# Optimization experiments

Measured on AMD Instinct MI355X. Metric: run time of the kernel, lower is better.

The kernel has to match this reference:

```python
import jax, jax.numpy as jnp
import numpy as np

VOCAB, D_MODEL, NHEAD, NLAYER, DIM_FF, MAX_LEN = 32000, 1024, 16, 6, 4096, 1024
B, L = 8, 1024
PAD_ID = 0
EPS = 1e-5


def _ln(x, g, b):
    m = x.mean(-1, keepdims=True)
    v = x.var(-1, keepdims=True)
    return (x - m) / jnp.sqrt(v + EPS) * g + b


def _mha(x, Wqkv, bqkv, Wo, bo, kpm):
    # x: [B,L,D]; Wqkv: [3D,D]; kpm: [B,L] bool (True = padded key)
    Bx, Lx, D = x.shape
    dh = D // NHEAD
    qkv = x @ Wqkv.T + bqkv                       # [B,L,3D]
    q, k, v = jnp.split(qkv, 3, axis=-1)
    sp = lambda t: t.reshape(Bx, Lx, NHEAD, dh).transpose(0, 2, 1, 3)  # [B,H,L,dh]
    q, k, v = sp(q), sp(k), sp(v)
    scores = jnp.einsum('bhqd,bhkd->bhqk', q, k) * (dh ** -0.5)
    scores = jnp.where(kpm[:, None, None, :], jnp.asarray(-1e9, scores.dtype), scores)
    attn = jax.nn.softmax(scores, axis=-1)        # explicit weights, as ForceWeightsMHA demands
    o = jnp.einsum('bhqk,bhkd->bhqd', attn, v)
    o = o.transpose(0, 2, 1, 3).reshape(Bx, Lx, D)
    return o @ Wo.T + bo


def setup_inputs() -> dict:
    key = jax.random.key(0)
    ks = jax.random.split(key, 20)
    s = 0.02
    n = lambda k, shp: (jax.random.normal(k, shp, dtype=jnp.float32) * s)
    inp = {
        'input_ids': jax.random.randint(ks[0], (B, L), 0, VOCAB, dtype=jnp.int64) if jax.config.jax_enable_x64 else jax.random.randint(ks[0], (B, L), 0, VOCAB).astype(jnp.int32),
        'tok_emb': n(ks[1], (VOCAB, D_MODEL)),
        'pos_emb': n(ks[2], (MAX_LEN, D_MODEL)),
        'Wqkv': n(ks[3], (NLAYER, 3 * D_MODEL, D_MODEL)),
        'bqkv': jnp.zeros((NLAYER, 3 * D_MODEL), jnp.float32),
        'Wo': n(ks[4], (NLAYER, D_MODEL, D_MODEL)),
        'bo': jnp.zeros((NLAYER, D_MODEL), jnp.float32),
        'ln1_g': jnp.ones((NLAYER, D_MODEL), jnp.float32),
        'ln1_b': jnp.zeros((NLAYER, D_MODEL), jnp.float32),
        'W1': n(ks[5], (NLAYER, DIM_FF, D_MODEL)),
        'b1': jnp.zeros((NLAYER, DIM_FF), jnp.float32),
        'W2': n(ks[6], (NLAYER, D_MODEL, DIM_FF)),
        'b2': jnp.zeros((NLAYER, D_MODEL), jnp.float32),
        'ln2_g': jnp.ones((NLAYER, D_MODEL), jnp.float32),
        'ln2_b': jnp.zeros((NLAYER, D_MODEL), jnp.float32),
        'head_ln_g': jnp.ones((D_MODEL,), jnp.float32),
        'head_ln_b': jnp.zeros((D_MODEL,), jnp.float32),
        'head_W': n(ks[7], (MAX_LEN, D_MODEL)),
        'head_b': jnp.zeros((MAX_LEN,), jnp.float32),
    }
    return inp


def reference(input_ids, tok_emb, pos_emb, Wqkv, bqkv, Wo, bo, ln1_g, ln1_b,
              W1, b1, W2, b2, ln2_g, ln2_b, head_ln_g, head_ln_b, head_W, head_b):
    Bx, Lx = input_ids.shape
    x = tok_emb[input_ids] + pos_emb[None, :Lx]           # [B,L,D]
    kpm = (input_ids == PAD_ID).at[:, 0].set(False)        # key padding mask, col 0 forced valid
    for i in range(NLAYER):                                # post-norm encoder layer (PyTorch default)
        x = _ln(x + _mha(x, Wqkv[i], bqkv[i], Wo[i], bo[i], kpm), ln1_g[i], ln1_b[i])
        ff = jax.nn.gelu(x @ W1[i].T + b1[i], approximate=False) @ W2[i].T + b2[i]
        x = _ln(x + ff, ln2_g[i], ln2_b[i])
    cls = x[:, 0, :]                                       # [B,D]
    return _ln(cls, head_ln_g, head_ln_b) @ head_W.T + head_b  # [B,MAX_LEN]
```

## Files before the change

kernel.cpp:

```cpp
#include <hip/hip_runtime.h>
#include <cstdint>

#define D_MODEL 1024
#define NHEAD   16
#define NLAYER  6
#define DIM_FF  4096
#define SEQ_B   8
#define SEQ_L   1024
#define TOKENS  (SEQ_B*SEQ_L)

typedef __bf16 v8bf __attribute__((ext_vector_type(8)));
typedef float  v4f  __attribute__((ext_vector_type(4)));

__device__ __forceinline__ unsigned short f2bf(float f) {
  unsigned int u = __float_as_uint(f);
  u += 0x7fffu + ((u >> 16) & 1u);
  return (unsigned short)(u >> 16);
}

__device__ __forceinline__ void gl_lds16(const void* g, void* l) {
  __builtin_amdgcn_global_load_lds(
      (const __attribute__((address_space(1))) void*)g,
      (__attribute__((address_space(3))) void*)l, 16, 0, 0);
}

__global__ __launch_bounds__(256) void f2b_kernel(const float* __restrict__ in,
                                                  unsigned short* __restrict__ out, long n) {
  long i = (long)blockIdx.x * 256 + threadIdx.x;
  long stride = (long)gridDim.x * 256;
  for (; i < n; i += stride) out[i] = f2bf(in[i]);
}

__global__ __launch_bounds__(256) void embed_kernel(const int* __restrict__ ids,
    const float* __restrict__ tok, const float* __restrict__ pos,
    float* __restrict__ X, unsigned short* __restrict__ Xb) {
  long i = (long)blockIdx.x * 256 + threadIdx.x;
  int d = (int)(i & (D_MODEL - 1));
  long bl = i >> 10;
  int l = (int)(bl & (SEQ_L - 1));
  int id = ids[bl];
  float v = tok[(long)id * D_MODEL + d] + pos[(long)l * D_MODEL + d];
  X[i] = v; Xb[i] = f2bf(v);
}

template<int EPI>
__global__ __launch_bounds__(256) void gemm128(
    const unsigned short* __restrict__ A,
    const unsigned short* __restrict__ W,
    const float* __restrict__ bias,
    float* __restrict__ Cf, unsigned short* __restrict__ Cb,
    unsigned short* __restrict__ Vt,
    int M, int N, int K) {
  __shared__ unsigned short As[128 * 32];
  __shared__ unsigned short Bs[128 * 32];
  int tid = threadIdx.x;
  int wave = tid >> 6, lane = tid & 63;
  int l15 = lane & 15, quad = lane >> 4;
  int m0 = blockIdx.y * 128, n0 = blockIdx.x * 128;
  int wm = (wave >> 1) * 64, wn = (wave & 1) * 64;

  int srow = tid >> 2, sc8 = (tid & 3) << 3;
  const unsigned short* Ag0 = A + (long)(m0 + srow) * K + sc8;
  const unsigned short* Ag1 = A + (long)(m0 + srow + 64) * K + sc8;
  const unsigned short* Wg0 = W + (long)(n0 + srow) * K + sc8;
  const unsigned short* Wg1 = W + (long)(n0 + srow + 64) * K + sc8;
  unsigned short* As0 = As + tid * 8;
  unsigned short* As1 = As + tid * 8 + 2048;
  unsigned short* Bs0 = Bs + tid * 8;
  unsigned short* Bs1 = Bs + tid * 8 + 2048;

  v4f acc[4][4];
  #pragma unroll
  for (int i = 0; i < 4; ++i)
    #pragma unroll
    for (int j = 0; j < 4; ++j) acc[i][j] = (v4f){0.f, 0.f, 0.f, 0.f};

  int ksteps = K >> 5;
  for (int ks = 0; ks < ksteps; ++ks) {
    int k0 = ks << 5;
    __syncthreads();
    gl_lds16(Ag0 + k0, As0);
    gl_lds16(Ag1 + k0, As1);
    gl_lds16(Wg0 + k0, Bs0);
    gl_lds16(Wg1 + k0, Bs1);
    __syncthreads();
    v8bf af[4], bf[4];
    #pragma unroll
    for (int i = 0; i < 4; ++i)
      af[i] = *(const v8bf*)&As[(wm + i * 16 + l15) * 32 + quad * 8];
    #pragma unroll
    for (int j = 0; j < 4; ++j)
      bf[j] = *(const v8bf*)&Bs[(wn + j * 16 + l15) * 32 + quad * 8];
    #pragma unroll
    for (int i = 0; i < 4; ++i)
      #pragma unroll
      for (int j = 0; j < 4; ++j)
        acc[i][j] = __builtin_amdgcn_mfma_f32_16x16x32_bf16(af[i], bf[j], acc[i][j], 0, 0, 0);
  }

  #pragma unroll
  for (int i = 0; i < 4; ++i) {
    int crow0 = m0 + wm + i * 16 + quad * 4;
    #pragma unroll
    for (int j = 0; j < 4; ++j) {
      int col = n0 + wn + j * 16 + l15;
      float bv = bias[col];
      if (EPI == 3 && col >= 2048) {
        int hc = (col - 2048) >> 6, d = (col - 2048) & 63;
        int bb = crow0 >> 10, l = crow0 & 1023;
        ushort4 pk;
        pk.x = f2bf(acc[i][j][0] + bv);
        pk.y = f2bf(acc[i][j][1] + bv);
        pk.z = f2bf(acc[i][j][2] + bv);
        pk.w = f2bf(acc[i][j][3] + bv);
        *(ushort4*)&Vt[((long)((bb * 16 + hc) * 64 + d)) * 1024 + l] = pk;
      } else {
        #pragma unroll
        for (int r = 0; r < 4; ++r) {
          float v = acc[i][j][r] + bv;
          if (EPI == 1) v = 0.5f * v * (1.f + erff(v * 0.70710678118f));
          long idx = (long)(crow0 + r) * N + col;
          if (EPI == 0) Cf[idx] = v;
          else          Cb[idx] = f2bf(v);
        }
      }
    }
  }
}

#define KP 72
__global__ __launch_bounds__(256) void attn2(
    const unsigned short* __restrict__ QKVb,
    const unsigned short* __restrict__ Vtg,
    const int* __restrict__ ids,
    unsigned short* __restrict__ Ob) {
  __shared__ unsigned short Ks[64 * KP];
  __shared__ unsigned short Vs[64 * KP];
  __shared__ unsigned short Ps[4][16 * KP];
  int tid = threadIdx.x, wave = tid >> 6, lane = tid & 63;
  int l15 = lane & 15, quad = lane >> 4;
  int b = blockIdx.z, h = blockIdx.y, q0 = blockIdx.x * 64;

  int qrow = q0 + wave * 16 + l15;
  const unsigned short* qb = QKVb + (long)(b * 1024 + qrow) * 3072 + h * 64;
  v8bf gq0 = *(const v8bf*)(qb + quad * 8);
  v8bf gq1 = *(const v8bf*)(qb + 32 + quad * 8);

  float m_run[4], l_run[4];
  v4f O[4];
  #pragma unroll
  for (int r = 0; r < 4; ++r) { m_run[r] = -1e30f; l_run[r] = 0.f; }
  #pragma unroll
  for (int j = 0; j < 4; ++j) O[j] = (v4f){0.f, 0.f, 0.f, 0.f};

  const unsigned short* kgb = QKVb + (long)b * 1024 * 3072 + 1024 + h * 64;
  const unsigned short* vgb = Vtg + (long)((b * 16 + h) * 64) * 1024;
  const int* idrow = ids + b * 1024;

  for (int k0 = 0; k0 < SEQ_L; k0 += 64) {
    __syncthreads();
    #pragma unroll
    for (int it = 0; it < 2; ++it) {
      int f = it * 256 + tid;
      int row = f >> 3, e8 = (f & 7) << 3;
      v8bf kv = *(const v8bf*)(kgb + (long)(k0 + row) * 3072 + e8);
      *(v8bf*)&Ks[row * KP + e8] = kv;
      v8bf vv = *(const v8bf*)(vgb + (long)row * 1024 + k0 + e8);
      *(v8bf*)&Vs[row * KP + e8] = vv;
    }
    __syncthreads();

    float p[4][4], mr[4];
    #pragma unroll
    for (int r = 0; r < 4; ++r) mr[r] = -1e30f;
    #pragma unroll
    for (int t = 0; t < 4; ++t) {
      v8bf kf0 = *(const v8bf*)&Ks[(t * 16 + l15) * KP + quad * 8];
      v8bf kf1 = *(const v8bf*)&Ks[(t * 16 + l15) * KP + 32 + quad * 8];
      v4f s = (v4f){0.f, 0.f, 0.f, 0.f};
      s = __builtin_amdgcn_mfma_f32_16x16x32_bf16(gq0, kf0, s, 0, 0, 0);
      s = __builtin_amdgcn_mfma_f32_16x16x32_bf16(gq1, kf1, s, 0, 0, 0);
      int kg = k0 + t * 16 + l15;
      bool msk = (idrow[kg] == 0) && (kg != 0);
      #pragma unroll
      for (int r = 0; r < 4; ++r) {
        float sv = msk ? -1e9f : s[r] * 0.125f;
        p[t][r] = sv;
        mr[r] = fmaxf(mr[r], sv);
      }
    }
    #pragma unroll
    for (int r = 0; r < 4; ++r) {
      mr[r] = fmaxf(mr[r], __shfl_xor(mr[r], 1, 64));
      mr[r] = fmaxf(mr[r], __shfl_xor(mr[r], 2, 64));
      mr[r] = fmaxf(mr[r], __shfl_xor(mr[r], 4, 64));
      mr[r] = fmaxf(mr[r], __shfl_xor(mr[r], 8, 64));
    }
    float alpha[4], ls[4];
    #pragma unroll
    for (int r = 0; r < 4; ++r) {
      float mn = fmaxf(m_run[r], mr[r]);
      alpha[r] = __expf(m_run[r] - mn);
      m_run[r] = mn; ls[r] = 0.f;
    }
    #pragma unroll
    for (int t = 0; t < 4; ++t)
      #pragma unroll
      for (int r = 0; r < 4; ++r) {
        p[t][r] = __expf(p[t][r] - m_run[r]);
        ls[r] += p[t][r];
      }
    #pragma unroll
    for (int r = 0; r < 4; ++r) {
      ls[r] += __shfl_xor(ls[r], 1, 64);
      ls[r] += __shfl_xor(ls[r], 2, 64);
      ls[r] += __shfl_xor(ls[r], 4, 64);
      ls[r] += __shfl_xor(ls[r], 8, 64);
      l_run[r] = l_run[r] * alpha[r] + ls[r];
    }
    #pragma unroll
    for (int j = 0; j < 4; ++j)
      #pragma unroll
      for (int r = 0; r < 4; ++r) O[j][r] *= alpha[r];

    #pragma unroll
    for (int t = 0; t < 4; ++t)
      #pragma unroll
      for (int r = 0; r < 4; ++r)
        Ps[wave][(quad * 4 + r) * KP + t * 16 + l15] = f2bf(p[t][r]);
    v8bf pa0 = *(const v8bf*)&Ps[wave][l15 * KP + quad * 8];
    v8bf pa1 = *(const v8bf*)&Ps[wave][l15 * KP + 32 + quad * 8];
    #pragma unroll
    for (int j = 0; j < 4; ++j) {
      v8bf vf0 = *(const v8bf*)&Vs[(j * 16 + l15) * KP + quad * 8];
      v8bf vf1 = *(const v8bf*)&Vs[(j * 16 + l15) * KP + 32 + quad * 8];
      O[j] = __builtin_amdgcn_mfma_f32_16x16x32_bf16(pa0, vf0, O[j], 0, 0, 0);
      O[j] = __builtin_amdgcn_mfma_f32_16x16x32_bf16(pa1, vf1, O[j], 0, 0, 0);
    }
  }

  int qd = q0 + wave * 16 + quad * 4;
  #pragma unroll
  for (int r = 0; r < 4; ++r) {
    float inv = 1.f / l_run[r];
    #pragma unroll
    for (int j = 0; j < 4; ++j)
      Ob[(long)(b * 1024 + qd + r) * 1024 + h * 64 + j * 16 + l15] = f2bf(O[j][r] * inv);
  }
}

__global__ __launch_bounds__(256) void add_ln(
    const float* __restrict__ Xin, const float* __restrict__ Yin,
    const float* __restrict__ g, const float* __restrict__ bta,
    float* __restrict__ outF, unsigned short* __restrict__ outB,
    long in_stride, long out_stride) {
  int row = blockIdx.x;
  const float* x = Xin + (long)row * in_stride;
  const float* y = Yin ? Yin + (long)row * 1024 : nullptr;
  int tid = threadIdx.x;
  float v[4];
  float s = 0.f, s2 = 0.f;
  #pragma unroll
  for (int j = 0; j < 4; ++j) {
    int d = j * 256 + tid;
    float t = x[d] + (y ? y[d] : 0.f);
    v[j] = t; s += t; s2 += t * t;
  }
  __shared__ float red[8];
  int lane = tid & 63, wave = tid >> 6;
  #pragma unroll
  for (int o = 32; o > 0; o >>= 1) { s += __shfl_down(s, o, 64); s2 += __shfl_down(s2, o, 64); }
  if (lane == 0) { red[wave] = s; red[4 + wave] = s2; }
  __syncthreads();
  s  = red[0] + red[1] + red[2] + red[3];
  s2 = red[4] + red[5] + red[6] + red[7];
  float mean = s * (1.f / 1024.f);
  float var  = s2 * (1.f / 1024.f) - mean * mean;
  float rstd = rsqrtf(var + 1e-5f);
  float* of = outF + (long)row * out_stride;
  unsigned short* ob = outB ? outB + (long)row * out_stride : nullptr;
  #pragma unroll
  for (int j = 0; j < 4; ++j) {
    int d = j * 256 + tid;
    float o = (v[j] - mean) * rstd * g[d] + bta[d];
    of[d] = o;
    if (ob) ob[d] = f2bf(o);
  }
}

__global__ __launch_bounds__(256) void head_kernel(
    const float* __restrict__ cls, const float* __restrict__ hW,
    const float* __restrict__ hb, float* __restrict__ out) {
  int n = blockIdx.x * 256 + threadIdx.x;
  int b = blockIdx.y;
  const float4* c4 = (const float4*)(cls + b * 1024);
  const float4* w4 = (const float4*)(hW + (long)n * 1024);
  float s = 0.f;
  #pragma unroll 8
  for (int d = 0; d < 256; ++d) {
    float4 a = c4[d], w = w4[d];
    s += a.x * w.x + a.y * w.y + a.z * w.z + a.w * w.w;
  }
  out[b * 1024 + n] = s + hb[n];
}

extern "C" void kernel_launch(void* const* d_in, const int* in_sizes, int n_in,
                              void* d_out, int out_size, void* d_ws, size_t ws_size,
                              hipStream_t stream) {
  const int*   ids  = (const int*)d_in[0];
  const float* tok  = (const float*)d_in[1];
  const float* pos  = (const float*)d_in[2];
  const float* Wqkv = (const float*)d_in[3];
  const float* bqkv = (const float*)d_in[4];
  const float* Wo   = (const float*)d_in[5];
  const float* bo   = (const float*)d_in[6];
  const float* ln1g = (const float*)d_in[7];
  const float* ln1b = (const float*)d_in[8];
  const float* W1   = (const float*)d_in[9];
  const float* b1   = (const float*)d_in[10];
  const float* W2   = (const float*)d_in[11];
  const float* b2   = (const float*)d_in[12];
  const float* ln2g = (const float*)d_in[13];
  const float* ln2b = (const float*)d_in[14];
  const float* hlng = (const float*)d_in[15];
  const float* hlnb = (const float*)d_in[16];
  const float* hW   = (const float*)d_in[17];
  const float* hb   = (const float*)d_in[18];
  float* out = (float*)d_out;

  char* ws = (char*)d_ws;
  size_t off = 0;
  auto alloc = [&](size_t bytes) {
    char* p = ws + off;
    off = (off + bytes + 255) & ~(size_t)255;
    return p;
  };
  unsigned short* Wqkv_b = (unsigned short*)alloc((size_t)NLAYER*3072*1024*2);
  unsigned short* Wo_b   = (unsigned short*)alloc((size_t)NLAYER*1024*1024*2);
  unsigned short* W1_b   = (unsigned short*)alloc((size_t)NLAYER*4096*1024*2);
  unsigned short* W2_b   = (unsigned short*)alloc((size_t)NLAYER*1024*4096*2);
  float*          X      = (float*)alloc((size_t)TOKENS*1024*4);
  unsigned short* Xb     = (unsigned short*)alloc((size_t)TOKENS*1024*2);
  unsigned short* Qb     = (unsigned short*)alloc((size_t)TOKENS*3072*2);
  unsigned short* Vtg    = (unsigned short*)alloc((size_t)TOKENS*1024*2);
  float*          Y      = (float*)alloc((size_t)TOKENS*1024*4);
  unsigned short* Ab     = (unsigned short*)alloc((size_t)TOKENS*1024*2);
  unsigned short* Gb     = Qb;
  float*          cls    = (float*)alloc(8*1024*4);

  f2b_kernel<<<2048, 256, 0, stream>>>(Wqkv, Wqkv_b, (long)NLAYER*3072*1024);
  f2b_kernel<<<2048, 256, 0, stream>>>(Wo,   Wo_b,   (long)NLAYER*1024*1024);
  f2b_kernel<<<2048, 256, 0, stream>>>(W1,   W1_b,   (long)NLAYER*4096*1024);
  f2b_kernel<<<2048, 256, 0, stream>>>(W2,   W2_b,   (long)NLAYER*1024*4096);
  embed_kernel<<<(TOKENS*1024)/256, 256, 0, stream>>>(ids, tok, pos, X, Xb);

  for (int i = 0; i < NLAYER; ++i) {
    gemm128<3><<<dim3(3072/128, TOKENS/128), 256, 0, stream>>>(
        Xb, Wqkv_b + (size_t)i*3072*1024, bqkv + i*3072, nullptr, Qb, Vtg, TOKENS, 3072, 1024);
    attn2<<<dim3(SEQ_L/64, NHEAD, SEQ_B), 256, 0, stream>>>(Qb, Vtg, ids, Ab);
    gemm128<0><<<dim3(1024/128, TOKENS/128), 256, 0, stream>>>(
        Ab, Wo_b + (size_t)i*1024*1024, bo + i*1024, Y, nullptr, nullptr, TOKENS, 1024, 1024);
    add_ln<<<TOKENS, 256, 0, stream>>>(X, Y, ln1g + i*1024, ln1b + i*1024, X, Xb, 1024L, 1024L);
    gemm128<1><<<dim3(4096/128, TOKENS/128), 256, 0, stream>>>(
        Xb, W1_b + (size_t)i*4096*1024, b1 + i*4096, nullptr, Gb, nullptr, TOKENS, 4096, 1024);
    gemm128<0><<<dim3(1024/128, TOKENS/128), 256, 0, stream>>>(
        Gb, W2_b + (size_t)i*1024*4096, b2 + i*1024, Y, nullptr, nullptr, TOKENS, 1024, 4096);
    add_ln<<<TOKENS, 256, 0, stream>>>(X, Y, ln2g + i*1024, ln2b + i*1024, X, Xb, 1024L, 1024L);
  }
  add_ln<<<8, 256, 0, stream>>>(X, nullptr, hlng, hlnb, cls, nullptr, (long)SEQ_L*1024, 1024L);
  head_kernel<<<dim3(4, 8), 256, 0, stream>>>(cls, hW, hb, out);
}
```

Measured before the change: 3.407 ms.

## Swizzle LDS tiles, remap GEMM blocks per XCD, streamline attention softmax

Applies an XOR swizzle to the GEMM A/B shared-memory tiles to avoid bank conflicts. It also remaps GEMM block indices so that each XCD works on a contiguous group of M tiles, for better L2 reuse. Attention now loads K/V straight into swizzled LDS with global_load_lds instead of a padded register copy. It precomputes an additive float mask bias and folds the softmax scale into an exp2 argument. The per-row probability sum is computed with an MFMA against a ones vector instead of shuffle reductions. Conversion and embedding kernels are vectorised to float4, and native bf16 conversions replace the manual rounding routine. The remap hardcodes the 64-tile M dimension, and the ones-MFMA row sum adds matrix work and a shuffle per tile.

```diff
diff --git a/kernel.cpp b/kernel.cpp
--- a/kernel.cpp
+++ b/kernel.cpp
@@ -9,14 +9,9 @@
 #define SEQ_L   1024
 #define TOKENS  (SEQ_B*SEQ_L)
 
-typedef __bf16 v8bf __attribute__((ext_vector_type(8)));
-typedef float  v4f  __attribute__((ext_vector_type(4)));
-
-__device__ __forceinline__ unsigned short f2bf(float f) {
-  unsigned int u = __float_as_uint(f);
-  u += 0x7fffu + ((u >> 16) & 1u);
-  return (unsigned short)(u >> 16);
-}
+typedef __bf16 v8bf  __attribute__((ext_vector_type(8)));
+typedef __bf16 v4bf  __attribute__((ext_vector_type(4)));
+typedef float  v4f   __attribute__((ext_vector_type(4)));
 
 __device__ __forceinline__ void gl_lds16(const void* g, void* l) {
   __builtin_amdgcn_global_load_lds(
@@ -24,23 +19,37 @@
       (__attribute__((address_space(3))) void*)l, 16, 0, 0);
 }
 
-__global__ __launch_bounds__(256) void f2b_kernel(const float* __restrict__ in,
-                                                  unsigned short* __restrict__ out, long n) {
+__global__ __launch_bounds__(256) void f2b_kernel(const float4* __restrict__ in,
+                                                  ushort4* __restrict__ out, long n4) {
   long i = (long)blockIdx.x * 256 + threadIdx.x;
   long stride = (long)gridDim.x * 256;
-  for (; i < n; i += stride) out[i] = f2bf(in[i]);
+  for (; i < n4; i += stride) {
+    float4 v = in[i];
+    v4bf r = { (__bf16)v.x, (__bf16)v.y, (__bf16)v.z, (__bf16)v.w };
+    out[i] = *(ushort4*)&r;
+  }
 }
 
 __global__ __launch_bounds__(256) void embed_kernel(const int* __restrict__ ids,
-    const float* __restrict__ tok, const float* __restrict__ pos,
-    float* __restrict__ X, unsigned short* __restrict__ Xb) {
+    const float4* __restrict__ tok, const float4* __restrict__ pos,
+    float4* __restrict__ X, ushort4* __restrict__ Xb) {
   long i = (long)blockIdx.x * 256 + threadIdx.x;
-  int d = (int)(i & (D_MODEL - 1));
-  long bl = i >> 10;
+  int d4 = (int)(i & 255);
+  long bl = i >> 8;
   int l = (int)(bl & (SEQ_L - 1));
   int id = ids[bl];
-  float v = tok[(long)id * D_MODEL + d] + pos[(long)l * D_MODEL + d];
-  X[i] = v; Xb[i] = f2bf(v);
+  float4 t = tok[(long)id * 256 + d4];
+  float4 p = pos[(long)l * 256 + d4];
+  float4 v = {t.x + p.x, t.y + p.y, t.z + p.z, t.w + p.w};
+  X[i] = v;
+  v4bf r = { (__bf16)v.x, (__bf16)v.y, (__bf16)v.z, (__bf16)v.w };
+  Xb[i] = *(ushort4*)&r;
+}
+
+__global__ __launch_bounds__(256) void maskb_kernel(const int* __restrict__ ids,
+                                                    float* __restrict__ mb) {
+  int i = blockIdx.x * 256 + threadIdx.x;
+  mb[i] = (ids[i] == 0 && (i & 1023) != 0) ? -1e9f : 0.f;
 }
 
 template<int EPI>
@@ -56,10 +65,17 @@
   int tid = threadIdx.x;
   int wave = tid >> 6, lane = tid & 63;
   int l15 = lane & 15, quad = lane >> 4;
-  int m0 = blockIdx.y * 128, n0 = blockIdx.x * 128;
+
+  int id = blockIdx.y * gridDim.x + blockIdx.x;
+  int xcd = id & 7, sidx = id >> 3;
+  int mt = xcd * 8 + (sidx & 7);
+  int nt = sidx >> 3;
+  int m0 = mt * 128, n0 = nt * 128;
   int wm = (wave >> 1) * 64, wn = (wave & 1) * 64;
 
-  int srow = tid >> 2, sc8 = (tid & 3) << 3;
+  int srow = tid >> 2;
+  int ssl  = (tid & 3) ^ ((srow >> 1) & 3);
+  int sc8  = ssl << 3;
   const unsigned short* Ag0 = A + (long)(m0 + srow) * K + sc8;
   const unsigned short* Ag1 = A + (long)(m0 + srow + 64) * K + sc8;
   const unsigned short* Wg0 = W + (long)(n0 + srow) * K + sc8;
@@ -68,6 +84,16 @@
   unsigned short* As1 = As + tid * 8 + 2048;
   unsigned short* Bs0 = Bs + tid * 8;
   unsigned short* Bs1 = Bs + tid * 8 + 2048;
+
+  const unsigned short* afp[4];
+  const unsigned short* bfp[4];
+  #pragma unroll
+  for (int i = 0; i < 4; ++i) {
+    int r = wm + i * 16 + l15;
+    afp[i] = &As[r * 32 + ((quad ^ ((r >> 1) & 3)) << 3)];
+    int rb = wn + i * 16 + l15;
+    bfp[i] = &Bs[rb * 32 + ((quad ^ ((rb >> 1) & 3)) << 3)];
+  }
 
   v4f acc[4][4];
   #pragma unroll
@@ -86,11 +112,9 @@
     __syncthreads();
     v8bf af[4], bf[4];
     #pragma unroll
-    for (int i = 0; i < 4; ++i)
-      af[i] = *(const v8bf*)&As[(wm + i * 16 + l15) * 32 + quad * 8];
-    #pragma unroll
-    for (int j = 0; j < 4; ++j)
-      bf[j] = *(const v8bf*)&Bs[(wn + j * 16 + l15) * 32 + quad * 8];
+    for (int i = 0; i < 4; ++i) af[i] = *(const v8bf*)afp[i];
+    #pragma unroll
+    for (int j = 0; j < 4; ++j) bf[j] = *(const v8bf*)bfp[j];
     #pragma unroll
     for (int i = 0; i < 4; ++i)
       #pragma unroll
@@ -108,12 +132,9 @@
       if (EPI == 3 && col >= 2048) {
         int hc = (col - 2048) >> 6, d = (col - 2048) & 63;
         int bb = crow0 >> 10, l = crow0 & 1023;
-        ushort4 pk;
-        pk.x = f2bf(acc[i][j][0] + bv);
-        pk.y = f2bf(acc[i][j][1] + bv);
-        pk.z = f2bf(acc[i][j][2] + bv);
-        pk.w = f2bf(acc[i][j][3] + bv);
-        *(ushort4*)&Vt[((long)((bb * 16 + hc) * 64 + d)) * 1024 + l] = pk;
+        v4bf pk = { (__bf16)(acc[i][j][0] + bv), (__bf16)(acc[i][j][1] + bv),
+                    (__bf16)(acc[i][j][2] + bv), (__bf16)(acc[i][j][3] + bv) };
+        *(ushort4*)&Vt[((long)((bb * 16 + hc) * 64 + d)) * 1024 + l] = *(ushort4*)&pk;
       } else {
         #pragma unroll
         for (int r = 0; r < 4; ++r) {
@@ -121,22 +142,22 @@
           if (EPI == 1) v = 0.5f * v * (1.f + erff(v * 0.70710678118f));
           long idx = (long)(crow0 + r) * N + col;
           if (EPI == 0) Cf[idx] = v;
-          else          Cb[idx] = f2bf(v);
+          else          ((__bf16*)Cb)[idx] = (__bf16)v;
         }
       }
     }
   }
 }
 
-#define KP 72
+#define PSP 72
 __global__ __launch_bounds__(256) void attn2(
     const unsigned short* __restrict__ QKVb,
     const unsigned short* __restrict__ Vtg,
-    const int* __restrict__ ids,
+    const float* __restrict__ mb,
     unsigned short* __restrict__ Ob) {
-  __shared__ unsigned short Ks[64 * KP];
-  __shared__ unsigned short Vs[64 * KP];
-  __shared__ unsigned short Ps[4][16 * KP];
+  __shared__ unsigned short Ks[64 * 64];
+  __shared__ unsigned short Vs[64 * 64];
+  __shared__ unsigned short Ps[4][16 * PSP];
   int tid = threadIdx.x, wave = tid >> 6, lane = tid & 63;
   int l15 = lane & 15, quad = lane >> 4;
   int b = blockIdx.z, h = blockIdx.y, q0 = blockIdx.x * 64;
@@ -146,6 +167,10 @@
   v8bf gq0 = *(const v8bf*)(qb + quad * 8);
   v8bf gq1 = *(const v8bf*)(qb + 32 + quad * 8);
 
+  v8bf bones;
+  #pragma unroll
+  for (int j = 0; j < 8; ++j) bones[j] = (l15 == 0) ? (__bf16)1.0f : (__bf16)0.0f;
+
   float m_run[4], l_run[4];
   v4f O[4];
   #pragma unroll
@@ -155,19 +180,20 @@
 
   const unsigned short* kgb = QKVb + (long)b * 1024 * 3072 + 1024 + h * 64;
   const unsigned short* vgb = Vtg + (long)((b * 16 + h) * 64) * 1024;
-  const int* idrow = ids + b * 1024;
+  const float* mrow = mb + b * 1024;
+
+  int srow = tid >> 3;
+  int ssl  = (tid & 7) ^ (srow & 7);
+  int ph0 = (quad ^ (l15 & 7)) << 3;
+  int ph1 = ((quad + 4) ^ (l15 & 7)) << 3;
+  const float SC = 0.18033688011112042f;
 
   for (int k0 = 0; k0 < SEQ_L; k0 += 64) {
     __syncthreads();
-    #pragma unroll
-    for (int it = 0; it < 2; ++it) {
-      int f = it * 256 + tid;
-      int row = f >> 3, e8 = (f & 7) << 3;
-      v8bf kv = *(const v8bf*)(kgb + (long)(k0 + row) * 3072 + e8);
-      *(v8bf*)&Ks[row * KP + e8] = kv;
-      v8bf vv = *(const v8bf*)(vgb + (long)row * 1024 + k0 + e8);
-      *(v8bf*)&Vs[row * KP + e8] = vv;
-    }
+    gl_lds16(kgb + (long)(k0 + srow) * 3072 + ssl * 8, &Ks[tid * 8]);
+    gl_lds16(kgb + (long)(k0 + srow + 32) * 3072 + ssl * 8, &Ks[tid * 8 + 2048]);
+    gl_lds16(vgb + (long)srow * 1024 + k0 + ssl * 8, &Vs[tid * 8]);
+    gl_lds16(vgb + (long)(srow + 32) * 1024 + k0 + ssl * 8, &Vs[tid * 8 + 2048]);
     __syncthreads();
 
     float p[4][4], mr[4];
@@ -175,16 +201,16 @@
     for (int r = 0; r < 4; ++r) mr[r] = -1e30f;
     #pragma unroll
     for (int t = 0; t < 4; ++t) {
-      v8bf kf0 = *(const v8bf*)&Ks[(t * 16 + l15) * KP + quad * 8];
-      v8bf kf1 = *(const v8bf*)&Ks[(t * 16 + l15) * KP + 32 + quad * 8];
+      int kr = t * 16 + l15;
+      v8bf kf0 = *(const v8bf*)&Ks[kr * 64 + ph0];
+      v8bf kf1 = *(const v8bf*)&Ks[kr * 64 + ph1];
       v4f s = (v4f){0.f, 0.f, 0.f, 0.f};
       s = __builtin_amdgcn_mfma_f32_16x16x32_bf16(gq0, kf0, s, 0, 0, 0);
       s = __builtin_amdgcn_mfma_f32_16x16x32_bf16(gq1, kf1, s, 0, 0, 0);
-      int kg = k0 + t * 16 + l15;
-      bool msk = (idrow[kg] == 0) && (kg != 0);
+      float bv = mrow[k0 + kr];
       #pragma unroll
       for (int r = 0; r < 4; ++r) {
-        float sv = msk ? -1e9f : s[r] * 0.125f;
+        float sv = fmaf(s[r], SC, bv);
         p[t][r] = sv;
         mr[r] = fmaxf(mr[r], sv);
       }
@@ -196,47 +222,45 @@
       mr[r] = fmaxf(mr[r], __shfl_xor(mr[r], 4, 64));
       mr[r] = fmaxf(mr[r], __shfl_xor(mr[r], 8, 64));
     }
-    float alpha[4], ls[4];
+    float alpha[4];
     #pragma unroll
     for (int r = 0; r < 4; ++r) {
       float mn = fmaxf(m_run[r], mr[r]);
-      alpha[r] = __expf(m_run[r] - mn);
-      m_run[r] = mn; ls[r] = 0.f;
+      alpha[r] = __builtin_amdgcn_exp2f(m_run[r] - mn);
+      m_run[r] = mn;
     }
     #pragma unroll
     for (int t = 0; t < 4; ++t)
       #pragma unroll
-      for (int r = 0; r < 4; ++r) {
-        p[t][r] = __expf(p[t][r] - m_run[r]);
-        ls[r] += p[t][r];
-      }
-    #pragma unroll
-    for (int r = 0; r < 4; ++r) {
-      ls[r] += __shfl_xor(ls[r], 1, 64);
-      ls[r] += __shfl_xor(ls[r], 2, 64);
-      ls[r] += __shfl_xor(ls[r], 4, 64);
-      ls[r] += __shfl_xor(ls[r], 8, 64);
-      l_run[r] = l_run[r] * alpha[r] + ls[r];
-    }
+      for (int r = 0; r < 4; ++r)
+        p[t][r] = __builtin_amdgcn_exp2f(p[t][r] - m_run[r]);
+
+    #pragma unroll
+    for (int t = 0; t < 4; ++t)
+      #pragma unroll
+      for (int r = 0; r < 4; ++r)
+        ((__bf16*)Ps[wave])[(quad * 4 + r) * PSP + t * 16 + l15] = (__bf16)p[t][r];
+    v8bf pa0 = *(const v8bf*)&Ps[wave][l15 * PSP + quad * 8];
+    v8bf pa1 = *(const v8bf*)&Ps[wave][l15 * PSP + 32 + quad * 8];
+
+    v4f ss = (v4f){0.f, 0.f, 0.f, 0.f};
+    ss = __builtin_amdgcn_mfma_f32_16x16x32_bf16(pa0, bones, ss, 0, 0, 0);
+    ss = __builtin_amdgcn_mfma_f32_16x16x32_bf16(pa1, bones, ss, 0, 0, 0);
+
     #pragma unroll
     for (int j = 0; j < 4; ++j)
       #pragma unroll
       for (int r = 0; r < 4; ++r) O[j][r] *= alpha[r];
-
-    #pragma unroll
-    for (int t = 0; t < 4; ++t)
-      #pragma unroll
-      for (int r = 0; r < 4; ++r)
-        Ps[wave][(quad * 4 + r) * KP + t * 16 + l15] = f2bf(p[t][r]);
-    v8bf pa0 = *(const v8bf*)&Ps[wave][l15 * KP + quad * 8];
-    v8bf pa1 = *(const v8bf*)&Ps[wave][l15 * KP + 32 + quad * 8];
     #pragma unroll
     for (int j = 0; j < 4; ++j) {
-      v8bf vf0 = *(const v8bf*)&Vs[(j * 16 + l15) * KP + quad * 8];
-      v8bf vf1 = *(const v8bf*)&Vs[(j * 16 + l15) * KP + 32 + quad * 8];
+      v8bf vf0 = *(const v8bf*)&Vs[(j * 16 + l15) * 64 + ph0];
+      v8bf vf1 = *(const v8bf*)&Vs[(j * 16 + l15) * 64 + ph1];
       O[j] = __builtin_amdgcn_mfma_f32_16x16x32_bf16(pa0, vf0, O[j], 0, 0, 0);
       O[j] = __builtin_amdgcn_mfma_f32_16x16x32_bf16(pa1, vf1, O[j], 0, 0, 0);
     }
+    #pragma unroll
+    for (int r = 0; r < 4; ++r)
+      l_run[r] = l_run[r] * alpha[r] + __shfl(ss[r], quad << 4, 64);
   }
 
   int qd = q0 + wave * 16 + quad * 4;
@@ -245,7 +269,8 @@
     float inv = 1.f / l_run[r];
     #pragma unroll
     for (int j = 0; j < 4; ++j)
-      Ob[(long)(b * 1024 + qd + r) * 1024 + h * 64 + j * 16 + l15] = f2bf(O[j][r] * inv);
+      ((__bf16*)Ob)[(long)(b * 1024 + qd + r) * 1024 + h * 64 + j * 16 + l15] =
+          (__bf16)(O[j][r] * inv);
   }
 }
 
@@ -284,7 +309,7 @@
     int d = j * 256 + tid;
     float o = (v[j] - mean) * rstd * g[d] + bta[d];
     of[d] = o;
-    if (ob) ob[d] = f2bf(o);
+    if (ob) ((__bf16*)ob)[d] = (__bf16)o;
   }
 }
 
@@ -347,17 +372,20 @@
   unsigned short* Ab     = (unsigned short*)alloc((size_t)TOKENS*1024*2);
   unsigned short* Gb     = Qb;
   float*          cls    = (float*)alloc(8*1024*4);
-
-  f2b_kernel<<<2048, 256, 0, stream>>>(Wqkv, Wqkv_b, (long)NLAYER*3072*1024);
-  f2b_kernel<<<2048, 256, 0, stream>>>(Wo,   Wo_b,   (long)NLAYER*1024*1024);
-  f2b_kernel<<<2048, 256, 0, stream>>>(W1,   W1_b,   (long)NLAYER*4096*1024);
-  f2b_kernel<<<2048, 256, 0, stream>>>(W2,   W2_b,   (long)NLAYER*1024*4096);
-  embed_kernel<<<(TOKENS*1024)/256, 256, 0, stream>>>(ids, tok, pos, X, Xb);
+  float*          mb     = (float*)alloc(TOKENS*4);
+
+  f2b_kernel<<<2048, 256, 0, stream>>>((const float4*)Wqkv, (ushort4*)Wqkv_b, (long)NLAYER*3072*1024/4);
+  f2b_kernel<<<2048, 256, 0, stream>>>((const float4*)Wo,   (ushort4*)Wo_b,   (long)NLAYER*1024*1024/4);
+  f2b_kernel<<<2048, 256, 0, stream>>>((const float4*)W1,   (ushort4*)W1_b,   (long)NLAYER*4096*1024/4);
+  f2b_kernel<<<2048, 256, 0, stream>>>((const float4*)W2,   (ushort4*)W2_b,   (long)NLAYER*1024*4096/4);
+  embed_kernel<<<(TOKENS*256)/256, 256, 0, stream>>>(ids, (const float4*)tok, (const float4*)pos,
+                                                     (float4*)X, (ushort4*)Xb);
+  maskb_kernel<<<TOKENS/256, 256, 0, stream>>>(ids, mb);
 
   for (int i = 0; i < NLAYER; ++i) {
     gemm128<3><<<dim3(3072/128, TOKENS/128), 256, 0, stream>>>(
         Xb, Wqkv_b + (size_t)i*3072*1024, bqkv + i*3072, nullptr, Qb, Vtg, TOKENS, 3072, 1024);
-    attn2<<<dim3(SEQ_L/64, NHEAD, SEQ_B), 256, 0, stream>>>(Qb, Vtg, ids, Ab);
+    attn2<<<dim3(SEQ_L/64, NHEAD, SEQ_B), 256, 0, stream>>>(Qb, Vtg, mb, Ab);
     gemm128<0><<<dim3(1024/128, TOKENS/128), 256, 0, stream>>>(
         Ab, Wo_b + (size_t)i*1024*1024, bo + i*1024, Y, nullptr, nullptr, TOKENS, 1024, 1024);
     add_ln<<<TOKENS, 256, 0, stream>>>(X, Y, ln1g + i*1024, ln1b + i*1024, X, Xb, 1024L, 1024L);
```

New measurement: 3.351 ms. Within noise of the previous version (-1.6%).
